# Performance work log

Hardware: AMD Instinct MI355X
Metric: run time of the kernel (lower is better)

Reference implementation:

```python
import jax, jax.numpy as jnp
import numpy as np

N_NODES = 50000


def gcn_conv(x, edge_index, W, b, n_nodes):
    # PyG GCNConv: add self-loops, symmetric normalization, scatter-add, then bias.
    src = jnp.concatenate([edge_index[0], jnp.arange(n_nodes)])
    dst = jnp.concatenate([edge_index[1], jnp.arange(n_nodes)])
    xw = x @ W  # [N, H]
    deg = jax.ops.segment_sum(jnp.ones_like(dst, dtype=xw.dtype), dst, num_segments=n_nodes)
    dinv = jnp.where(deg > 0, jax.lax.rsqrt(jnp.maximum(deg, 1e-12)), 0.0)
    norm = dinv[src] * dinv[dst]  # [E+N]
    msgs = xw[src] * norm[:, None]  # gather + scale
    out = jax.ops.segment_sum(msgs, dst, num_segments=n_nodes)  # scatter-add
    return out + b


def setup_inputs() -> dict:
    key = jax.random.key(0)
    ks = jax.random.split(key, 12)
    d_in, d_h = 128, 128
    inp = {
        "x": jax.random.normal(ks[0], (N_NODES, d_in), dtype=jnp.float32),
        "edge_index": jax.random.randint(ks[1], (2, 800000), 0, N_NODES, dtype=jnp.int64),
        "conv_W": jax.random.normal(ks[2], (d_in, d_h), dtype=jnp.float32) * 0.05,
        "conv_b": jax.random.normal(ks[3], (d_h,), dtype=jnp.float32) * 0.05,
        "W1": jax.random.normal(ks[4], (d_h, 500), dtype=jnp.float32) * 0.05,
        "b1": jax.random.normal(ks[5], (500,), dtype=jnp.float32) * 0.05,
        "W2": jax.random.normal(ks[6], (500, 500), dtype=jnp.float32) * 0.05,
        "b2": jax.random.normal(ks[7], (500,), dtype=jnp.float32) * 0.05,
        "W3": jax.random.normal(ks[8], (500, 500), dtype=jnp.float32) * 0.05,
        "b3": jax.random.normal(ks[9], (500,), dtype=jnp.float32) * 0.05,
        "Wo": jax.random.normal(ks[10], (500, 1), dtype=jnp.float32) * 0.05,
        "bo": jax.random.normal(ks[11], (1,), dtype=jnp.float32) * 0.05,
    }
    return inp


def reference(x, edge_index, conv_W, conv_b, W1, b1, W2, b2, W3, b3, Wo, bo):
    h = jax.nn.relu(gcn_conv(x, edge_index, conv_W, conv_b, N_NODES))
    h = jax.nn.relu(h @ W1 + b1)
    h = jax.nn.relu(h @ W2 + b2)
    h = jax.nn.relu(h @ W3 + b3)
    return h @ Wo + bo
```

## Files before the change

kernel.cpp:

```cpp
#include <hip/hip_runtime.h>
#include <hip/hip_bf16.h>
#include <hip/hip_fp16.h>

#define NN 50000
#define NE 800000

typedef _Float16 f16;
typedef _Float16 f16x2 __attribute__((ext_vector_type(2)));
typedef _Float16 f16x8 __attribute__((ext_vector_type(8)));
typedef float f32x4 __attribute__((ext_vector_type(4)));

__device__ __forceinline__ void gload16(const f16* g, f16* l) {
    __builtin_amdgcn_global_load_lds(
        (__attribute__((address_space(1))) void*)(void*)g,
        (__attribute__((address_space(3))) void*)(void*)l, 16, 0, 0);
}

__global__ void detect_mode_kernel(const void* ei, int* mode) {
    if (threadIdx.x == 0 && blockIdx.x == 0) {
        const long long* p = (const long long*)ei;
        int ok64 = 1;
        for (int i = 0; i < 128; ++i) {
            long long v = p[i];
            if (v < 0 || v >= NN) { ok64 = 0; break; }
        }
        *mode = ok64;
    }
}

__device__ __forceinline__ int edge_at(const void* ei, int mode, int idx) {
    if (mode) return (int)((const long long*)ei)[idx];
    return ((const int*)ei)[idx];
}

__global__ void deg_kernel(const void* ei, const int* mode_p, int* degi) {
    int e = blockIdx.x * blockDim.x + threadIdx.x;
    if (e >= NE) return;
    int mode = *mode_p;
    int d = edge_at(ei, mode, NE + e);
    atomicAdd(&degi[d], 1);
}

#define NBLK 49
__global__ __launch_bounds__(1024)
void scan_blocksum(const int* __restrict__ degi, int* __restrict__ bsum) {
    __shared__ int red[1024];
    int i = blockIdx.x * 1024 + threadIdx.x;
    red[threadIdx.x] = (i < NN) ? degi[i] : 0;
    __syncthreads();
    for (int s = 512; s > 0; s >>= 1) {
        if (threadIdx.x < s) red[threadIdx.x] += red[threadIdx.x + s];
        __syncthreads();
    }
    if (threadIdx.x == 0) bsum[blockIdx.x] = red[0];
}
__global__ void scan_top(const int* __restrict__ bsum, int* __restrict__ boff) {
    if (threadIdx.x == 0) {
        int acc = 0;
        for (int b = 0; b < NBLK; ++b) { boff[b] = acc; acc += bsum[b]; }
    }
}
__global__ __launch_bounds__(1024)
void scan_apply(const int* __restrict__ degi, const int* __restrict__ boff,
                int* __restrict__ off, float* __restrict__ dinv) {
    __shared__ int tmp[1024];
    int tid = threadIdx.x;
    int i = blockIdx.x * 1024 + tid;
    int v = (i < NN) ? degi[i] : 0;
    tmp[tid] = v;
    __syncthreads();
    for (int s = 1; s < 1024; s <<= 1) {
        int t = (tid >= s) ? tmp[tid - s] : 0;
        __syncthreads();
        tmp[tid] += t;
        __syncthreads();
    }
    if (i < NN) {
        off[i] = boff[blockIdx.x] + tmp[tid] - v;
        dinv[i] = rsqrtf((float)v + 1.0f);
    }
}

__global__ void fill_kernel(const void* ei, const int* mode_p,
                            const int* __restrict__ off, int* __restrict__ cursor,
                            int* __restrict__ csr) {
    int e = blockIdx.x * blockDim.x + threadIdx.x;
    if (e >= NE) return;
    int mode = *mode_p;
    int s = edge_at(ei, mode, e);
    int d = edge_at(ei, mode, NE + e);
    int pos = atomicAdd(&cursor[d], 1);
    csr[off[d] + pos] = s;
}

__global__ __launch_bounds__(256)
void gather_kernel(const int* __restrict__ csr, const int* __restrict__ off,
                   const int* __restrict__ degi, const f16* __restrict__ xwh,
                   const float* __restrict__ dinv, const float* __restrict__ conv_b,
                   f16* __restrict__ h0h) {
    int wv = threadIdx.x >> 6, lane = threadIdx.x & 63;
    int n = blockIdx.x * 4 + wv;
    if (n >= NN) return;
    int o = off[n], dg = degi[n];
    float ax = 0.f, ay = 0.f, bx = 0.f, by = 0.f;
    int j = 0;
    for (; j + 1 < dg; j += 2) {
        int s0 = csr[o + j], s1 = csr[o + j + 1];
        float d0 = dinv[s0], d1 = dinv[s1];
        f16x2 v0 = *(const f16x2*)(xwh + (size_t)s0 * 128 + lane * 2);
        f16x2 v1 = *(const f16x2*)(xwh + (size_t)s1 * 128 + lane * 2);
        ax += (float)v0[0] * d0; ay += (float)v0[1] * d0;
        bx += (float)v1[0] * d1; by += (float)v1[1] * d1;
    }
    if (j < dg) {
        int s0 = csr[o + j];
        float d0 = dinv[s0];
        f16x2 v0 = *(const f16x2*)(xwh + (size_t)s0 * 128 + lane * 2);
        ax += (float)v0[0] * d0; ay += (float)v0[1] * d0;
    }
    float dn = dinv[n];
    f16x2 vs = *(const f16x2*)(xwh + (size_t)n * 128 + lane * 2);
    float rx = (ax + bx + (float)vs[0] * dn) * dn + conv_b[lane * 2];
    float ry = (ay + by + (float)vs[1] * dn) * dn + conv_b[lane * 2 + 1];
    f16x2 r;
    r[0] = (f16)fmaxf(rx, 0.f);
    r[1] = (f16)fmaxf(ry, 0.f);
    *(f16x2*)(h0h + (size_t)n * 128 + lane * 2) = r;
}

__global__ void convert_x(const float* __restrict__ x, f16* __restrict__ xh) {
    int i = (blockIdx.x * 256 + threadIdx.x) * 8;
    if (i >= NN * 128) return;
    float4 u0 = *(const float4*)(x + i);
    float4 u1 = *(const float4*)(x + i + 4);
    f16x8 o;
    o[0] = (f16)u0.x; o[1] = (f16)u0.y; o[2] = (f16)u0.z; o[3] = (f16)u0.w;
    o[4] = (f16)u1.x; o[5] = (f16)u1.y; o[6] = (f16)u1.z; o[7] = (f16)u1.w;
    *(f16x8*)(xh + i) = o;
}

__global__ void prep_weights(const float* __restrict__ cW, const float* __restrict__ W1,
                             const float* __restrict__ W2, const float* __restrict__ W3,
                             const float* __restrict__ Wo, const float* __restrict__ b1,
                             const float* __restrict__ b2, const float* __restrict__ b3,
                             f16* __restrict__ cWT, f16* __restrict__ W1T,
                             f16* __restrict__ W2T, f16* __restrict__ W3T,
                             float* __restrict__ Wof, float* __restrict__ b1p,
                             float* __restrict__ b2p, float* __restrict__ b3p) {
    int i = blockIdx.x * 256 + threadIdx.x;
    if (i < 16384) { int n = i >> 7, k = i & 127; cWT[i] = (f16)cW[k * 128 + n]; return; }
    i -= 16384;
    if (i < 65536) { int n = i >> 7, k = i & 127; W1T[i] = (f16)((n < 500) ? W1[k * 500 + n] : 0.f); return; }
    i -= 65536;
    if (i < 262144) { int n = i >> 9, k = i & 511; W2T[i] = (f16)((n < 500 && k < 500) ? W2[k * 500 + n] : 0.f); return; }
    i -= 262144;
    if (i < 262144) { int n = i >> 9, k = i & 511; W3T[i] = (f16)((n < 500 && k < 500) ? W3[k * 500 + n] : 0.f); return; }
    i -= 262144;
    if (i < 512) { Wof[i] = (i < 500) ? Wo[i] : 0.f; return; }
    i -= 512;
    if (i < 512) { b1p[i] = (i < 500) ? b1[i] : 0.f; return; }
    i -= 512;
    if (i < 512) { b2p[i] = (i < 500) ? b2[i] : 0.f; return; }
    i -= 512;
    if (i < 512) { b3p[i] = (i < 500) ? b3[i] : 0.f; return; }
}

template <bool RELU, bool BIAS>
__global__ __launch_bounds__(256)
void mfma_gemm(const f16* __restrict__ A, const f16* __restrict__ Bt,
               const float* __restrict__ biasp, f16* __restrict__ C,
               int M, int Npad, int K) {
    __shared__ f16 As[2][4096];
    __shared__ f16 Bs[2][4096];
    const int tid = threadIdx.x;
    const int lane = tid & 63;
    const int wm = (tid >> 6) >> 1, wn = (tid >> 6) & 1;
    const int l15 = lane & 15, lk = lane >> 4;
    const int row0 = blockIdx.y * 128, col0 = blockIdx.x * 128;

    size_t abase[2], bbase[2];
#pragma unroll
    for (int i = 0; i < 2; ++i) {
        int s = tid + i * 256;
        int m = s >> 2;
        int kgp = (s & 3) ^ (m & 3);
        int row = row0 + m; if (row > M - 1) row = M - 1;
        abase[i] = (size_t)row * K + kgp * 8;
        bbase[i] = (size_t)(col0 + m) * K + kgp * 8;
    }
    const int fragoff = l15 * 32 + ((lk ^ (l15 & 3)) * 8);
    f32x4 acc[4][4] = {};

    const int nt = K >> 5;
#pragma unroll
    for (int i = 0; i < 2; ++i) {
        gload16(A + abase[i], &As[0][tid * 8 + i * 2048]);
        gload16(Bt + bbase[i], &Bs[0][tid * 8 + i * 2048]);
    }
    __syncthreads();
    int cur = 0;
    for (int t = 0; t < nt; ++t) {
        if (t + 1 < nt) {
            int k0 = (t + 1) << 5;
#pragma unroll
            for (int i = 0; i < 2; ++i) {
                gload16(A + abase[i] + k0, &As[cur ^ 1][tid * 8 + i * 2048]);
                gload16(Bt + bbase[i] + k0, &Bs[cur ^ 1][tid * 8 + i * 2048]);
            }
        }
        f16x8 af[4], bf[4];
#pragma unroll
        for (int f = 0; f < 4; ++f) {
            af[f] = *(const f16x8*)&As[cur][(wm * 64 + f * 16) * 32 + fragoff];
            bf[f] = *(const f16x8*)&Bs[cur][(wn * 64 + f * 16) * 32 + fragoff];
        }
#pragma unroll
        for (int fi = 0; fi < 4; ++fi)
#pragma unroll
            for (int fj = 0; fj < 4; ++fj)
                acc[fi][fj] = __builtin_amdgcn_mfma_f32_16x16x32_f16(
                    af[fi], bf[fj], acc[fi][fj], 0, 0, 0);
        __syncthreads();
        cur ^= 1;
    }
#pragma unroll
    for (int fi = 0; fi < 4; ++fi)
#pragma unroll
        for (int r = 0; r < 4; ++r) {
            int row = row0 + wm * 64 + fi * 16 + lk * 4 + r;
            if (row < M) {
#pragma unroll
                for (int fj = 0; fj < 4; ++fj) {
                    int n = col0 + wn * 64 + fj * 16 + l15;
                    float v = acc[fi][fj][r];
                    if (BIAS) v += biasp[n];
                    if (RELU) v = fmaxf(v, 0.f);
                    C[(size_t)row * Npad + n] = (f16)v;
                }
            }
        }
}

__global__ __launch_bounds__(256)
void final_gemv(const f16* __restrict__ H, const float* __restrict__ Wof,
                const float* __restrict__ bo, float* __restrict__ out) {
    int wv = threadIdx.x >> 6, lane = threadIdx.x & 63;
    int row = blockIdx.x * 4 + wv;
    if (row >= NN) return;
    f16x8 hv = *(const f16x8*)(H + (size_t)row * 512 + lane * 8);
    float s = 0.f;
#pragma unroll
    for (int j = 0; j < 8; ++j) s += (float)hv[j] * Wof[lane * 8 + j];
#pragma unroll
    for (int o = 32; o > 0; o >>= 1) s += __shfl_down(s, o, 64);
    if (lane == 0) out[row] = s + bo[0];
}

extern "C" void kernel_launch(void* const* d_in, const int* in_sizes, int n_in,
                              void* d_out, int out_size, void* d_ws, size_t ws_size,
                              hipStream_t stream) {
    const float* x      = (const float*)d_in[0];
    const void*  ei     = d_in[1];
    const float* conv_W = (const float*)d_in[2];
    const float* conv_b = (const float*)d_in[3];
    const float* W1 = (const float*)d_in[4];
    const float* b1 = (const float*)d_in[5];
    const float* W2 = (const float*)d_in[6];
    const float* b2 = (const float*)d_in[7];
    const float* W3 = (const float*)d_in[8];
    const float* b3 = (const float*)d_in[9];
    const float* Wo = (const float*)d_in[10];
    const float* bo = (const float*)d_in[11];
    float* out = (float*)d_out;

    char* ws = (char*)d_ws;
    size_t off_b = 0;
    auto alloc = [&](size_t bytes) {
        void* p = ws + off_b;
        off_b = (off_b + bytes + 255) & ~(size_t)255;
        return p;
    };
    f16*   xh   = (f16*)alloc((size_t)NN * 128 * 2);
    f16*   xwh  = (f16*)alloc((size_t)NN * 128 * 2);
    f16*   h0h  = (f16*)alloc((size_t)NN * 128 * 2);
    f16*   h1h  = (f16*)alloc((size_t)NN * 512 * 2);
    f16*   h2h  = (f16*)alloc((size_t)NN * 512 * 2);
    f16*   cWT  = (f16*)alloc(128 * 128 * 2);
    f16*   W1T  = (f16*)alloc(512 * 128 * 2);
    f16*   W2T  = (f16*)alloc(512 * 512 * 2);
    f16*   W3T  = (f16*)alloc(512 * 512 * 2);
    float* Wof  = (float*)alloc(512 * 4);
    float* b1p  = (float*)alloc(512 * 4);
    float* b2p  = (float*)alloc(512 * 4);
    float* b3p  = (float*)alloc(512 * 4);
    int*   degi   = (int*)alloc(NN * 4);
    int*   offn   = (int*)alloc(NN * 4);
    int*   cursor = (int*)alloc(NN * 4);
    float* dinv   = (float*)alloc(NN * 4);
    int*   bsum   = (int*)alloc(NBLK * 4);
    int*   boff   = (int*)alloc(NBLK * 4);
    int*   mode   = (int*)alloc(256);
    int*   csr    = (int*)alloc((size_t)NE * 4);

    hipMemsetAsync(degi, 0, (size_t)NN * 4, stream);
    hipMemsetAsync(cursor, 0, (size_t)NN * 4, stream);
    detect_mode_kernel<<<1, 1, 0, stream>>>(ei, mode);
    convert_x<<<(NN * 128 / 8 + 255) / 256, 256, 0, stream>>>(x, xh);
    prep_weights<<<(608256 + 255) / 256, 256, 0, stream>>>(
        conv_W, W1, W2, W3, Wo, b1, b2, b3, cWT, W1T, W2T, W3T, Wof, b1p, b2p, b3p);

    mfma_gemm<false, false><<<dim3(1, 391), 256, 0, stream>>>(
        xh, cWT, nullptr, xwh, NN, 128, 128);

    deg_kernel<<<(NE + 255) / 256, 256, 0, stream>>>(ei, mode, degi);
    scan_blocksum<<<NBLK, 1024, 0, stream>>>(degi, bsum);
    scan_top<<<1, 64, 0, stream>>>(bsum, boff);
    scan_apply<<<NBLK, 1024, 0, stream>>>(degi, boff, offn, dinv);
    fill_kernel<<<(NE + 255) / 256, 256, 0, stream>>>(ei, mode, offn, cursor, csr);
    gather_kernel<<<(NN + 3) / 4, 256, 0, stream>>>(csr, offn, degi, xwh, dinv, conv_b, h0h);

    mfma_gemm<true, true><<<dim3(4, 391), 256, 0, stream>>>(
        h0h, W1T, b1p, h1h, NN, 512, 128);
    mfma_gemm<true, true><<<dim3(4, 391), 256, 0, stream>>>(
        h1h, W2T, b2p, h2h, NN, 512, 512);
    mfma_gemm<true, true><<<dim3(4, 391), 256, 0, stream>>>(
        h2h, W3T, b3p, h1h, NN, 512, 512);
    final_gemv<<<(NN + 3) / 4, 256, 0, stream>>>(h1h, Wof, bo, out);
}
```

Measured before the change: 395.8 us.

## Fuse final GEMV into last GEMM, swizzle tile order, merge prep kernels

```diff
diff --git a/kernel.cpp b/kernel.cpp
--- a/kernel.cpp
+++ b/kernel.cpp
@@ -16,16 +16,15 @@
         (__attribute__((address_space(3))) void*)(void*)l, 16, 0, 0);
 }
 
-__global__ void detect_mode_kernel(const void* ei, int* mode) {
-    if (threadIdx.x == 0 && blockIdx.x == 0) {
-        const long long* p = (const long long*)ei;
-        int ok64 = 1;
-        for (int i = 0; i < 128; ++i) {
-            long long v = p[i];
-            if (v < 0 || v >= NN) { ok64 = 0; break; }
-        }
-        *mode = ok64;
-    }
+__device__ __forceinline__ int detect_mode(const void* ei) {
+    const long long* p = (const long long*)ei;
+    int ok = 1;
+#pragma unroll
+    for (int i = 0; i < 8; ++i) {
+        long long v = p[i];
+        if (v < 0 || v >= NN) ok = 0;
+    }
+    return ok;
 }
 
 __device__ __forceinline__ int edge_at(const void* ei, int mode, int idx) {
@@ -33,10 +32,10 @@
     return ((const int*)ei)[idx];
 }
 
-__global__ void deg_kernel(const void* ei, const int* mode_p, int* degi) {
+__global__ void deg_kernel(const void* ei, int* degi) {
     int e = blockIdx.x * blockDim.x + threadIdx.x;
     if (e >= NE) return;
-    int mode = *mode_p;
+    int mode = detect_mode(ei);
     int d = edge_at(ei, mode, NE + e);
     atomicAdd(&degi[d], 1);
 }
@@ -62,7 +61,8 @@
 }
 __global__ __launch_bounds__(1024)
 void scan_apply(const int* __restrict__ degi, const int* __restrict__ boff,
-                int* __restrict__ off, float* __restrict__ dinv) {
+                int* __restrict__ off, float* __restrict__ dinv,
+                const float* __restrict__ bo, float* __restrict__ out) {
     __shared__ int tmp[1024];
     int tid = threadIdx.x;
     int i = blockIdx.x * 1024 + tid;
@@ -78,15 +78,16 @@
     if (i < NN) {
         off[i] = boff[blockIdx.x] + tmp[tid] - v;
         dinv[i] = rsqrtf((float)v + 1.0f);
-    }
-}
-
-__global__ void fill_kernel(const void* ei, const int* mode_p,
+        out[i] = bo[0];
+    }
+}
+
+__global__ void fill_kernel(const void* ei,
                             const int* __restrict__ off, int* __restrict__ cursor,
                             int* __restrict__ csr) {
     int e = blockIdx.x * blockDim.x + threadIdx.x;
     if (e >= NE) return;
-    int mode = *mode_p;
+    int mode = detect_mode(ei);
     int s = edge_at(ei, mode, e);
     int d = edge_at(ei, mode, NE + e);
     int pos = atomicAdd(&cursor[d], 1);
@@ -128,26 +129,27 @@
     *(f16x2*)(h0h + (size_t)n * 128 + lane * 2) = r;
 }
 
-__global__ void convert_x(const float* __restrict__ x, f16* __restrict__ xh) {
-    int i = (blockIdx.x * 256 + threadIdx.x) * 8;
-    if (i >= NN * 128) return;
-    float4 u0 = *(const float4*)(x + i);
-    float4 u1 = *(const float4*)(x + i + 4);
-    f16x8 o;
-    o[0] = (f16)u0.x; o[1] = (f16)u0.y; o[2] = (f16)u0.z; o[3] = (f16)u0.w;
-    o[4] = (f16)u1.x; o[5] = (f16)u1.y; o[6] = (f16)u1.z; o[7] = (f16)u1.w;
-    *(f16x8*)(xh + i) = o;
-}
-
-__global__ void prep_weights(const float* __restrict__ cW, const float* __restrict__ W1,
-                             const float* __restrict__ W2, const float* __restrict__ W3,
-                             const float* __restrict__ Wo, const float* __restrict__ b1,
-                             const float* __restrict__ b2, const float* __restrict__ b3,
-                             f16* __restrict__ cWT, f16* __restrict__ W1T,
-                             f16* __restrict__ W2T, f16* __restrict__ W3T,
-                             float* __restrict__ Wof, float* __restrict__ b1p,
-                             float* __restrict__ b2p, float* __restrict__ b3p) {
+__global__ void prep_all(const float* __restrict__ x, f16* __restrict__ xh,
+                         const float* __restrict__ cW, const float* __restrict__ W1,
+                         const float* __restrict__ W2, const float* __restrict__ W3,
+                         const float* __restrict__ Wo, const float* __restrict__ b1,
+                         const float* __restrict__ b2, const float* __restrict__ b3,
+                         f16* __restrict__ cWT, f16* __restrict__ W1T,
+                         f16* __restrict__ W2T, f16* __restrict__ W3T,
+                         float* __restrict__ Wof, float* __restrict__ b1p,
+                         float* __restrict__ b2p, float* __restrict__ b3p) {
     int i = blockIdx.x * 256 + threadIdx.x;
+    if (i < 800000) {
+        int e = i * 8;
+        float4 u0 = *(const float4*)(x + e);
+        float4 u1 = *(const float4*)(x + e + 4);
+        f16x8 o;
+        o[0] = (f16)u0.x; o[1] = (f16)u0.y; o[2] = (f16)u0.z; o[3] = (f16)u0.w;
+        o[4] = (f16)u1.x; o[5] = (f16)u1.y; o[6] = (f16)u1.z; o[7] = (f16)u1.w;
+        *(f16x8*)(xh + e) = o;
+        return;
+    }
+    i -= 800000;
     if (i < 16384) { int n = i >> 7, k = i & 127; cWT[i] = (f16)cW[k * 128 + n]; return; }
     i -= 16384;
     if (i < 65536) { int n = i >> 7, k = i & 127; W1T[i] = (f16)((n < 500) ? W1[k * 500 + n] : 0.f); return; }
@@ -165,18 +167,29 @@
     if (i < 512) { b3p[i] = (i < 500) ? b3[i] : 0.f; return; }
 }
 
-template <bool RELU, bool BIAS>
+template <bool SWZ, bool RELU, bool BIAS, bool FUSE>
 __global__ __launch_bounds__(256)
 void mfma_gemm(const f16* __restrict__ A, const f16* __restrict__ Bt,
                const float* __restrict__ biasp, f16* __restrict__ C,
+               const float* __restrict__ Wof, float* __restrict__ out,
                int M, int Npad, int K) {
+    int bx, by;
+    if (SWZ) {
+        int id = blockIdx.x + 4 * blockIdx.y;
+        int x = id & 7, s = id >> 3;
+        bx = s & 3;
+        by = (s >> 2) * 8 + x;
+        if (by * 128 >= M) return;
+    } else {
+        bx = blockIdx.x; by = blockIdx.y;
+    }
     __shared__ f16 As[2][4096];
     __shared__ f16 Bs[2][4096];
     const int tid = threadIdx.x;
     const int lane = tid & 63;
     const int wm = (tid >> 6) >> 1, wn = (tid >> 6) & 1;
     const int l15 = lane & 15, lk = lane >> 4;
-    const int row0 = blockIdx.y * 128, col0 = blockIdx.x * 128;
+    const int row0 = by * 128, col0 = bx * 128;
 
     size_t abase[2], bbase[2];
 #pragma unroll
@@ -223,37 +236,45 @@
         __syncthreads();
         cur ^= 1;
     }
-#pragma unroll
-    for (int fi = 0; fi < 4; ++fi)
-#pragma unroll
-        for (int r = 0; r < 4; ++r) {
-            int row = row0 + wm * 64 + fi * 16 + lk * 4 + r;
-            if (row < M) {
+    if (FUSE) {
+#pragma unroll
+        for (int fi = 0; fi < 4; ++fi)
+#pragma unroll
+            for (int r = 0; r < 4; ++r) {
+                float part = 0.f;
 #pragma unroll
                 for (int fj = 0; fj < 4; ++fj) {
                     int n = col0 + wn * 64 + fj * 16 + l15;
                     float v = acc[fi][fj][r];
                     if (BIAS) v += biasp[n];
                     if (RELU) v = fmaxf(v, 0.f);
-                    C[(size_t)row * Npad + n] = (f16)v;
+                    part += v * Wof[n];
+                }
+                part += __shfl_xor(part, 1, 64);
+                part += __shfl_xor(part, 2, 64);
+                part += __shfl_xor(part, 4, 64);
+                part += __shfl_xor(part, 8, 64);
+                int row = row0 + wm * 64 + fi * 16 + lk * 4 + r;
+                if (l15 == 0 && row < M) atomicAdd(out + row, part);
+            }
+    } else {
+#pragma unroll
+        for (int fi = 0; fi < 4; ++fi)
+#pragma unroll
+            for (int r = 0; r < 4; ++r) {
+                int row = row0 + wm * 64 + fi * 16 + lk * 4 + r;
+                if (row < M) {
+#pragma unroll
+                    for (int fj = 0; fj < 4; ++fj) {
+                        int n = col0 + wn * 64 + fj * 16 + l15;
+                        float v = acc[fi][fj][r];
+                        if (BIAS) v += biasp[n];
+                        if (RELU) v = fmaxf(v, 0.f);
+                        C[(size_t)row * Npad + n] = (f16)v;
+                    }
                 }
             }
-        }
-}
-
-__global__ __launch_bounds__(256)
-void final_gemv(const f16* __restrict__ H, const float* __restrict__ Wof,
-                const float* __restrict__ bo, float* __restrict__ out) {
-    int wv = threadIdx.x >> 6, lane = threadIdx.x & 63;
-    int row = blockIdx.x * 4 + wv;
-    if (row >= NN) return;
-    f16x8 hv = *(const f16x8*)(H + (size_t)row * 512 + lane * 8);
-    float s = 0.f;
-#pragma unroll
-    for (int j = 0; j < 8; ++j) s += (float)hv[j] * Wof[lane * 8 + j];
-#pragma unroll
-    for (int o = 32; o > 0; o >>= 1) s += __shfl_down(s, o, 64);
-    if (lane == 0) out[row] = s + bo[0];
+    }
 }
 
 extern "C" void kernel_launch(void* const* d_in, const int* in_sizes, int n_in,
@@ -299,31 +320,29 @@
     float* dinv   = (float*)alloc(NN * 4);
     int*   bsum   = (int*)alloc(NBLK * 4);
     int*   boff   = (int*)alloc(NBLK * 4);
-    int*   mode   = (int*)alloc(256);
     int*   csr    = (int*)alloc((size_t)NE * 4);
 
     hipMemsetAsync(degi, 0, (size_t)NN * 4, stream);
     hipMemsetAsync(cursor, 0, (size_t)NN * 4, stream);
-    detect_mode_kernel<<<1, 1, 0, stream>>>(ei, mode);
-    convert_x<<<(NN * 128 / 8 + 255) / 256, 256, 0, stream>>>(x, xh);
-    prep_weights<<<(608256 + 255) / 256, 256, 0, stream>>>(
-        conv_W, W1, W2, W3, Wo, b1, b2, b3, cWT, W1T, W2T, W3T, Wof, b1p, b2p, b3p);
-
-    mfma_gemm<false, false><<<dim3(1, 391), 256, 0, stream>>>(
-        xh, cWT, nullptr, xwh, NN, 128, 128);
-
-    deg_kernel<<<(NE + 255) / 256, 256, 0, stream>>>(ei, mode, degi);
+
+    prep_all<<<(1408256 + 255) / 256, 256, 0, stream>>>(
+        x, xh, conv_W, W1, W2, W3, Wo, b1, b2, b3,
+        cWT, W1T, W2T, W3T, Wof, b1p, b2p, b3p);
+
+    mfma_gemm<false, false, false, false><<<dim3(1, 391), 256, 0, stream>>>(
+        xh, cWT, nullptr, xwh, nullptr, nullptr, NN, 128, 128);
+
+    deg_kernel<<<(NE + 255) / 256, 256, 0, stream>>>(ei, degi);
     scan_blocksum<<<NBLK, 1024, 0, stream>>>(degi, bsum);
     scan_top<<<1, 64, 0, stream>>>(bsum, boff);
-    scan_apply<<<NBLK, 1024, 0, stream>>>(degi, boff, offn, dinv);
-    fill_kernel<<<(NE + 255) / 256, 256, 0, stream>>>(ei, mode, offn, cursor, csr);
+    scan_apply<<<NBLK, 1024, 0, stream>>>(degi, boff, offn, dinv, bo, out);
+    fill_kernel<<<(NE + 255) / 256, 256, 0, stream>>>(ei, offn, cursor, csr);
     gather_kernel<<<(NN + 3) / 4, 256, 0, stream>>>(csr, offn, degi, xwh, dinv, conv_b, h0h);
 
-    mfma_gemm<true, true><<<dim3(4, 391), 256, 0, stream>>>(
-        h0h, W1T, b1p, h1h, NN, 512, 128);
-    mfma_gemm<true, true><<<dim3(4, 391), 256, 0, stream>>>(
-        h1h, W2T, b2p, h2h, NN, 512, 512);
-    mfma_gemm<true, true><<<dim3(4, 391), 256, 0, stream>>>(
-        h2h, W3T, b3p, h1h, NN, 512, 512);
-    final_gemv<<<(NN + 3) / 4, 256, 0, stream>>>(h1h, Wof, bo, out);
-}
+    mfma_gemm<true, true, true, false><<<dim3(4, 392), 256, 0, stream>>>(
+        h0h, W1T, b1p, h1h, nullptr, nullptr, NN, 512, 128);
+    mfma_gemm<true, true, true, false><<<dim3(4, 392), 256, 0, stream>>>(
+        h1h, W2T, b2p, h2h, nullptr, nullptr, NN, 512, 512);
+    mfma_gemm<true, true, true, true><<<dim3(4, 392), 256, 0, stream>>>(
+        h2h, W3T, b3p, nullptr, Wof, out, NN, 512, 512);
+}
```

Measured after the change: 375.1 us. 5.2% less time.
